# Optimization experiments

Measured on AMD Instinct MI355X. Metric: run time of the kernel, lower is better.

The kernel has to match this reference:

```python
import jax, jax.numpy as jnp
import numpy as np

EPS = 1e-5
K = 20

def knn_idx(x, k):
    # x: (B, N, C) -> (B, N, k) indices of k nearest neighbors (negative sq-dist top-k, self included)
    sq = jnp.sum(x * x, axis=-1)                      # (B, N)
    inner = jnp.einsum('bnc,bmc->bnm', x, x)          # (B, N, N)
    neg_dist = 2.0 * inner - sq[:, :, None] - sq[:, None, :]
    _, idx = jax.lax.top_k(neg_dist, k)
    return idx

def edge_conv(x, w, g, b, m, v, k):
    # x: (B, N, C); w: (O, 2C); BN eval-mode params over O
    idx = knn_idx(x, k)                               # (B, N, k)
    nb = jax.vmap(lambda f, i: f[i])(x, idx)          # (B, N, k, C)
    ctr = x[:, :, None, :]
    e = jnp.concatenate([nb - ctr, jnp.broadcast_to(ctr, nb.shape)], axis=-1)  # (B,N,k,2C)
    h = jnp.einsum('bnkc,oc->bnko', e, w)
    h = (h - m) * jax.lax.rsqrt(v + EPS) * g + b
    h = jnp.where(h > 0, h, 0.2 * h)                  # LeakyReLU(0.2)
    return jnp.max(h, axis=2)                         # (B, N, O)

def conv1d_bn_relu(x, w, bias, g, bt, m, v):
    h = jnp.einsum('bnc,oc->bno', x, w) + bias
    h = (h - m) * jax.lax.rsqrt(v + EPS) * g + bt
    return jax.nn.relu(h)

def setup_inputs() -> dict:
    key = jax.random.key(0)
    ks = jax.random.split(key, 16)
    B, N = 2, 4096
    d = {'x': jax.random.normal(ks[0], (B, N, 3), dtype=jnp.float32)}
    dims = [(3, 64), (64, 64), (64, 128), (128, 256)]
    for i, (ci, co) in enumerate(dims, start=1):
        d[f'w{i}'] = jax.random.normal(ks[i], (co, 2 * ci), dtype=jnp.float32) * 0.05
        d[f'g{i}'] = jnp.ones((co,), jnp.float32)
        d[f'bt{i}'] = jnp.zeros((co,), jnp.float32)
        d[f'm{i}'] = jnp.zeros((co,), jnp.float32)
        d[f'v{i}'] = jnp.ones((co,), jnp.float32)
    head = [(512, 256), (256, 128)]
    for i, (ci, co) in enumerate(head, start=1):
        d[f'hw{i}'] = jax.random.normal(ks[8 + i], (co, ci), dtype=jnp.float32) * 0.05
        d[f'hb{i}'] = jnp.zeros((co,), jnp.float32)
        d[f'hg{i}'] = jnp.ones((co,), jnp.float32)
        d[f'hbt{i}'] = jnp.zeros((co,), jnp.float32)
        d[f'hm{i}'] = jnp.zeros((co,), jnp.float32)
        d[f'hv{i}'] = jnp.ones((co,), jnp.float32)
    d['hw3'] = jax.random.normal(ks[12], (1, 128), dtype=jnp.float32) * 0.05
    d['hb3'] = jnp.zeros((1,), jnp.float32)
    return d

def reference(x, w1, g1, bt1, m1, v1, w2, g2, bt2, m2, v2, w3, g3, bt3, m3, v3,
              w4, g4, bt4, m4, v4,
              hw1, hb1, hg1, hbt1, hm1, hv1, hw2, hb2, hg2, hbt2, hm2, hv2, hw3, hb3):
    x1 = edge_conv(x, w1, g1, bt1, m1, v1, K)   # (B, N, 64)
    x2 = edge_conv(x1, w2, g2, bt2, m2, v2, K)  # (B, N, 64)
    x3 = edge_conv(x2, w3, g3, bt3, m3, v3, K)  # (B, N, 128)
    x4 = edge_conv(x3, w4, g4, bt4, m4, v4, K)  # (B, N, 256)
    xc = jnp.concatenate([x1, x2, x3, x4], axis=-1)  # (B, N, 512)
    h = conv1d_bn_relu(xc, hw1, hb1, hg1, hbt1, hm1, hv1)
    h = conv1d_bn_relu(h, hw2, hb2, hg2, hbt2, hm2, hv2)
    out = jnp.einsum('bnc,oc->bno', h, hw3) + hb3    # (B, N, 1)
    return out[..., 0]                               # (B, N)
```

## Files before the change

kernel.cpp:

```cpp
#include <hip/hip_runtime.h>

#define NPTS 4096
#define EPSF 1e-5f

__device__ __forceinline__ unsigned f2u(float f) {
  unsigned b = __float_as_uint(f);
  return (b & 0x80000000u) ? ~b : (b | 0x80000000u);
}
__device__ __forceinline__ float u2f(unsigned u) {
  unsigned b = (u & 0x80000000u) ? (u & 0x7fffffffu) : ~u;
  return __uint_as_float(b);
}
__device__ __forceinline__ unsigned shflx(unsigned v, int j) {
  return (unsigned)__shfl_xor((int)v, j);
}
__device__ __forceinline__ unsigned long long shflx64(unsigned long long v, int j) {
  unsigned lo = (unsigned)__shfl_xor((int)(unsigned)(v & 0xffffffffull), j);
  unsigned hi = (unsigned)__shfl_xor((int)(unsigned)(v >> 32), j);
  return ((unsigned long long)hi << 32) | lo;
}

__device__ __forceinline__ unsigned sort64_u32(unsigned v, int lane) {
#pragma unroll
  for (int k = 2; k <= 64; k <<= 1) {
#pragma unroll
    for (int j = k >> 1; j >= 1; j >>= 1) {
      unsigned ov = shflx(v, j);
      bool kmin = ((lane & j) == 0) == ((lane & k) == 0);
      v = kmin ? (v < ov ? v : ov) : (v > ov ? v : ov);
    }
  }
  return v;
}

__device__ __forceinline__ void sort128_u32(unsigned& a, unsigned& b, int lane) {
#pragma unroll
  for (int k = 2; k <= 128; k <<= 1) {
#pragma unroll
    for (int j = k >> 1; j >= 1; j >>= 1) {
      if (j == 64) {
        unsigned mn = a < b ? a : b, mx = a < b ? b : a;
        a = mn; b = mx;
      } else {
        unsigned oa = shflx(a, j), ob = shflx(b, j);
        bool lower = (lane & j) == 0;
        bool asca, ascb;
        if (k == 128) { asca = true; ascb = true; }
        else if (k == 64) { asca = true; ascb = false; }
        else { asca = ((lane & k) == 0); ascb = asca; }
        a = (lower == asca) ? (a < oa ? a : oa) : (a > oa ? a : oa);
        b = (lower == ascb) ? (b < ob ? b : ob) : (b > ob ? b : ob);
      }
    }
  }
}

__device__ __forceinline__ unsigned long long sort64_u64(unsigned long long v, int lane) {
#pragma unroll
  for (int k = 2; k <= 64; k <<= 1) {
#pragma unroll
    for (int j = k >> 1; j >= 1; j >>= 1) {
      unsigned long long ov = shflx64(v, j);
      bool kmin = ((lane & j) == 0) == ((lane & k) == 0);
      v = kmin ? (v < ov ? v : ov) : (v > ov ? v : ov);
    }
  }
  return v;
}

__device__ __forceinline__ void sort128_u64(unsigned long long& a, unsigned long long& b,
                                            int lane) {
#pragma unroll
  for (int k = 2; k <= 128; k <<= 1) {
#pragma unroll
    for (int j = k >> 1; j >= 1; j >>= 1) {
      if (j == 64) {
        unsigned long long mn = a < b ? a : b, mx = a < b ? b : a;
        a = mn; b = mx;
      } else {
        unsigned long long oa = shflx64(a, j), ob = shflx64(b, j);
        bool lower = (lane & j) == 0;
        bool asca, ascb;
        if (k == 128) { asca = true; ascb = true; }
        else if (k == 64) { asca = true; ascb = false; }
        else { asca = ((lane & k) == 0); ascb = asca; }
        a = (lower == asca) ? (a < oa ? a : oa) : (a > oa ? a : oa);
        b = (lower == ascb) ? (b < ob ? b : ob) : (b > ob ? b : ob);
      }
    }
  }
}

struct TopkShared {
  unsigned wv[80];
  unsigned ck[128];
  int      ci[128];
  int      cnt_s;
  int      selm[20];
  float    part[4 * 256];
  float    fcv[80];
  int      fcm[80];
};

__device__ __forceinline__ void topk_select(float v[16], TopkShared& sh,
                                            int tid, int lane, int wid) {
  float M = v[0];
#pragma unroll
  for (int j = 1; j < 16; ++j) M = fmaxf(M, v[j]);

  unsigned mk = sort64_u32(f2u(M), lane);

  if (tid == 0) sh.cnt_s = 0;
  if (lane >= 44) sh.wv[wid * 20 + (63 - lane)] = mk;
  __syncthreads();

  unsigned a0 = sh.wv[lane];
  unsigned b0 = (lane < 16) ? sh.wv[64 + lane] : 0u;
  sort128_u32(a0, b0, lane);
  unsigned T0k = (unsigned)__shfl((int)b0, 44);
  float T0f = u2f(T0k);

#pragma unroll
  for (int j = 0; j < 16; ++j) {
    bool pred = (v[j] >= T0f);
    unsigned long long m = __ballot(pred);
    int below = __popcll(m & ((1ull << lane) - 1ull));
    int cw = __popcll(m);
    int base = 0;
    if (lane == 0 && cw) base = atomicAdd(&sh.cnt_s, cw);
    base = __shfl(base, 0);
    if (pred) {
      int pos = base + below;
      if (pos < 128) { sh.ck[pos] = f2u(v[j]); sh.ci[pos] = j * 256 + tid; }
    }
  }
  __syncthreads();
  const int cnt = sh.cnt_s;

  if (cnt <= 128) {
    unsigned long long k0 = (lane < cnt)
        ? (((unsigned long long)sh.ck[lane] << 32) | (unsigned)(~sh.ci[lane])) : 0ull;
    if (cnt <= 64) {
      k0 = sort64_u64(k0, lane);
      if (wid == 0 && lane >= 44) sh.selm[63 - lane] = (int)(~(unsigned)k0);
    } else {
      unsigned long long k1 = (64 + lane < cnt)
          ? (((unsigned long long)sh.ck[64 + lane] << 32) | (unsigned)(~sh.ci[64 + lane]))
          : 0ull;
      sort128_u64(k0, k1, lane);
      if (wid == 0 && lane >= 44) sh.selm[63 - lane] = (int)(~(unsigned)k1);
    }
  } else {
    for (int it = 0; it < 20; ++it) {
      float bv = v[0]; int bj = 0;
#pragma unroll
      for (int j = 1; j < 16; ++j)
        if (v[j] > bv) { bv = v[j]; bj = j; }
      int bm = bj * 256 + tid;
#pragma unroll
      for (int off = 1; off < 64; off <<= 1) {
        float ov = __shfl_xor(bv, off);
        int om = __shfl_xor(bm, off);
        if (ov > bv || (ov == bv && om < bm)) { bv = ov; bm = om; }
      }
      if (lane == 0) { sh.fcv[wid * 20 + it] = bv; sh.fcm[wid * 20 + it] = bm; }
      if ((bm & 255) == tid) v[bm >> 8] = -3.0e38f;
    }
    __syncthreads();
    if (wid == 0) {
      float c0 = sh.fcv[lane]; int m0 = sh.fcm[lane];
      float c1 = (lane < 16) ? sh.fcv[64 + lane] : -3.0e38f;
      int   m1 = (lane < 16) ? sh.fcm[64 + lane] : 0x7fffffff;
      for (int it = 0; it < 20; ++it) {
        float bv; int bm, bs;
        if (c0 > c1 || (c0 == c1 && m0 < m1)) { bv = c0; bm = m0; bs = lane; }
        else { bv = c1; bm = m1; bs = 64 + lane; }
#pragma unroll
        for (int off = 1; off < 64; off <<= 1) {
          float ov = __shfl_xor(bv, off);
          int om = __shfl_xor(bm, off);
          int os = __shfl_xor(bs, off);
          if (ov > bv || (ov == bv && om < bm)) { bv = ov; bm = om; bs = os; }
        }
        if (lane == 0) sh.selm[it] = bm;
        if (bs == lane) c0 = -3.0e38f;
        else if (bs == 64 + lane) c1 = -3.0e38f;
      }
    }
  }
  __syncthreads();
}

__device__ __forceinline__ void topk_gather(const TopkShared& sh, TopkShared& shm,
                                            const float* __restrict__ P,
                                            const float* __restrict__ Q,
                                            float* __restrict__ Y, int ldy, int O,
                                            int bBase, int n, int tid, int lane, int wid) {
  for (int o = lane; o < O; o += 64) {
    float q = Q[(size_t)(bBase + n) * O + o];
    float best = -3.0e38f;
#pragma unroll
    for (int kk = 0; kk < 5; ++kk) {
      int s = sh.selm[wid * 5 + kk];
      float t = P[(size_t)(bBase + s) * O + o] + q;
      t = t > 0.f ? t : 0.2f * t;
      best = fmaxf(best, t);
    }
    shm.part[wid * 256 + o] = best;
  }
  __syncthreads();
  for (int o = tid; o < O; o += 256) {
    float b2 = fmaxf(fmaxf(shm.part[o], shm.part[256 + o]),
                     fmaxf(shm.part[512 + o], shm.part[768 + o]));
    Y[(size_t)(bBase + n) * ldy + o] = b2;
  }
}

__global__ void fold_edge_k(const float* __restrict__ w, const float* __restrict__ g,
                            const float* __restrict__ bt, const float* __restrict__ m,
                            const float* __restrict__ v, int O, int C,
                            float* __restrict__ wdf, float* __restrict__ wqf,
                            float* __restrict__ c0) {
  int t = blockIdx.x * 256 + threadIdx.x;
  if (t >= O * C) return;
  int o = t / C, c = t - o * C;
  float A = g[o] * (1.0f / sqrtf(v[o] + EPSF));
  float wd = w[o * 2 * C + c], wc = w[o * 2 * C + C + c];
  wdf[t] = A * wd;
  wqf[t] = A * (wc - wd);
  if (c == 0) c0[o] = bt[o] - m[o] * A;
}

__global__ void fold_head_k(const float* __restrict__ hw, const float* __restrict__ hb,
                            const float* __restrict__ hg, const float* __restrict__ hbt,
                            const float* __restrict__ hm, const float* __restrict__ hv,
                            int O, int C, float* __restrict__ hwf, float* __restrict__ cb) {
  int t = blockIdx.x * 256 + threadIdx.x;
  if (t >= O * C) return;
  int o = t / C, c = t - o * C;
  float A = hg[o] * (1.0f / sqrtf(hv[o] + EPSF));
  hwf[t] = A * hw[t];
  if (c == 0) cb[o] = (hb[o] - hm[o]) * A + hbt[o];
}

__global__ void sq_k(const float* __restrict__ X, int lda, int C,
                     float* __restrict__ sq, int nrows) {
  int r = blockIdx.x * 256 + threadIdx.x;
  if (r >= nrows) return;
  const float* p = X + (size_t)r * lda;
  float s = 0.f;
  for (int c = 0; c < C; ++c) s += p[c] * p[c];
  sq[r] = s;
}

__global__ void pq3_k(const float* __restrict__ x, const float* __restrict__ wdf,
                      const float* __restrict__ wqf, const float* __restrict__ c0,
                      float* __restrict__ P, float* __restrict__ Q) {
  int t = blockIdx.x * 256 + threadIdx.x;
  int r = t >> 6, o = t & 63;
  float x0 = x[r * 3], x1 = x[r * 3 + 1], x2 = x[r * 3 + 2];
  P[(size_t)r * 64 + o] = x0 * wdf[o * 3] + x1 * wdf[o * 3 + 1] + x2 * wdf[o * 3 + 2];
  Q[(size_t)r * 64 + o] = x0 * wqf[o * 3] + x1 * wqf[o * 3 + 1] + x2 * wqf[o * 3 + 2] + c0[o];
}

__global__ void dist3_k(const float* __restrict__ xb, const float* __restrict__ sqb,
                        float* __restrict__ D, int r0) {
  int t = blockIdx.x * 256 + threadIdx.x;
  int rl = t >> 12;
  int mc = t & (NPTS - 1);
  int n = r0 + rl;
  float x0 = xb[n * 3], x1 = xb[n * 3 + 1], x2 = xb[n * 3 + 2];
  float y0 = xb[mc * 3], y1 = xb[mc * 3 + 1], y2 = xb[mc * 3 + 2];
  float inner = x0 * y0 + x1 * y1 + x2 * y2;
  D[(size_t)rl * NPTS + mc] = 2.0f * inner - sqb[n] - sqb[mc];
}

__global__ __launch_bounds__(256) void topk_l1_fused(
    const float* __restrict__ x, const float* __restrict__ sqg,
    const float* __restrict__ P, const float* __restrict__ Q,
    float* __restrict__ Y, int ldy) {
  const int tid = threadIdx.x;
  const int lane = tid & 63, wid = tid >> 6;
  const int n = blockIdx.x;
  const int bBase = blockIdx.y * NPTS;
  const float* xb = x + (size_t)bBase * 3;
  const float* sqb = sqg + bBase;

  __shared__ TopkShared sh;

  float xn0 = xb[n * 3], xn1 = xb[n * 3 + 1], xn2 = xb[n * 3 + 2];
  float sn = sqb[n];
  float v[16];
#pragma unroll
  for (int j = 0; j < 16; ++j) {
    int mc = j * 256 + tid;
    float y0 = xb[mc * 3], y1 = xb[mc * 3 + 1], y2 = xb[mc * 3 + 2];
    float inner = xn0 * y0 + xn1 * y1 + xn2 * y2;
    v[j] = 2.0f * inner - sn - sqb[mc];
  }

  topk_select(v, sh, tid, lane, wid);
  topk_gather(sh, sh, P, Q, Y, ldy, 64, bBase, n, tid, lane, wid);
}

__global__ __launch_bounds__(256) void dist_sym_k(
    const float* __restrict__ X0, int lda, int C,
    const float* __restrict__ sq0, float* __restrict__ D0) {
  int t = blockIdx.x;
  int bi = 0;
  while (t >= 32 - bi) { t -= 32 - bi; ++bi; }
  const int bj = bi + t;
  const int b = blockIdx.y;
  const float* X = X0 + (size_t)b * NPTS * lda;
  const float* sq = sq0 + (size_t)b * NPTS;
  float* D = D0 + (size_t)b * NPTS * NPTS;

  const int row0 = bi * 128, col0 = bj * 128;
  const int tid = threadIdx.x;
  const int tx = tid & 15, ty = tid >> 4;

  __shared__ float As[16 * 132];
  __shared__ float Bs[16 * 132];

  const int lr = tid >> 1;
  const int lc = (tid & 1) * 8;
  const float* Ap = X + (size_t)(row0 + lr) * lda + lc;
  const float* Bp = X + (size_t)(col0 + lr) * lda + lc;

  float acc[8][8] = {};
  for (int c0 = 0; c0 < C; c0 += 16) {
    float4 a0 = *(const float4*)(Ap + c0);
    float4 a1 = *(const float4*)(Ap + c0 + 4);
    float4 b0 = *(const float4*)(Bp + c0);
    float4 b1 = *(const float4*)(Bp + c0 + 4);
    __syncthreads();
    As[(lc + 0) * 132 + lr] = a0.x; As[(lc + 1) * 132 + lr] = a0.y;
    As[(lc + 2) * 132 + lr] = a0.z; As[(lc + 3) * 132 + lr] = a0.w;
    As[(lc + 4) * 132 + lr] = a1.x; As[(lc + 5) * 132 + lr] = a1.y;
    As[(lc + 6) * 132 + lr] = a1.z; As[(lc + 7) * 132 + lr] = a1.w;
    Bs[(lc + 0) * 132 + lr] = b0.x; Bs[(lc + 1) * 132 + lr] = b0.y;
    Bs[(lc + 2) * 132 + lr] = b0.z; Bs[(lc + 3) * 132 + lr] = b0.w;
    Bs[(lc + 4) * 132 + lr] = b1.x; Bs[(lc + 5) * 132 + lr] = b1.y;
    Bs[(lc + 6) * 132 + lr] = b1.z; Bs[(lc + 7) * 132 + lr] = b1.w;
    __syncthreads();
#pragma unroll
    for (int c = 0; c < 16; ++c) {
      float4 av0 = *(const float4*)&As[c * 132 + ty * 8];
      float4 av1 = *(const float4*)&As[c * 132 + ty * 8 + 4];
      float4 bv0 = *(const float4*)&Bs[c * 132 + tx * 8];
      float4 bv1 = *(const float4*)&Bs[c * 132 + tx * 8 + 4];
      float aa[8] = {av0.x, av0.y, av0.z, av0.w, av1.x, av1.y, av1.z, av1.w};
      float bb[8] = {bv0.x, bv0.y, bv0.z, bv0.w, bv1.x, bv1.y, bv1.z, bv1.w};
#pragma unroll
      for (int i = 0; i < 8; ++i)
#pragma unroll
        for (int j = 0; j < 8; ++j) acc[i][j] = fmaf(aa[i], bb[j], acc[i][j]);
    }
  }

  float rs[8], cs[8];
#pragma unroll
  for (int i = 0; i < 8; ++i) rs[i] = sq[row0 + ty * 8 + i];
#pragma unroll
  for (int j = 0; j < 8; ++j) cs[j] = sq[col0 + tx * 8 + j];

#pragma unroll
  for (int i = 0; i < 8; ++i) {
    const int row = row0 + ty * 8 + i;
    float vals[8];
#pragma unroll
    for (int j = 0; j < 8; ++j) vals[j] = (2.0f * acc[i][j] - rs[i]) - cs[j];
    *(float4*)&D[(size_t)row * NPTS + col0 + tx * 8] =
        make_float4(vals[0], vals[1], vals[2], vals[3]);
    *(float4*)&D[(size_t)row * NPTS + col0 + tx * 8 + 4] =
        make_float4(vals[4], vals[5], vals[6], vals[7]);
  }

  if (bi != bj) {
#pragma unroll
    for (int j = 0; j < 8; ++j) {
      const int col = col0 + tx * 8 + j;
      float mv[8];
#pragma unroll
      for (int i = 0; i < 8; ++i) mv[i] = (2.0f * acc[i][j] - cs[j]) - rs[i];
      *(float4*)&D[(size_t)col * NPTS + row0 + ty * 8] =
          make_float4(mv[0], mv[1], mv[2], mv[3]);
      *(float4*)&D[(size_t)col * NPTS + row0 + ty * 8 + 4] =
          make_float4(mv[4], mv[5], mv[6], mv[7]);
    }
  }
}

template <int EPI>
__global__ __launch_bounds__(256) void gemm_nt(
    const float* __restrict__ A, int lda,
    const float* __restrict__ Bm, int ldb,
    float* __restrict__ Out, int ldo, int C,
    const float* __restrict__ sqA, const float* __restrict__ sqB,
    const float* __restrict__ bias) {
  __shared__ __align__(16) float As[16][68];
  __shared__ __align__(16) float Bs[16][68];
  const int tx = threadIdx.x, ty = threadIdx.y;
  const int tid = ty * 16 + tx;
  const int row0 = blockIdx.y * 64, col0 = blockIdx.x * 64;
  const int lr = tid >> 2;
  const int lc = (tid & 3) << 2;
  const float* Ap = A + (size_t)(row0 + lr) * lda + lc;
  const float* Bp = Bm + (size_t)(col0 + lr) * ldb + lc;
  float acc[4][4] = {};
  for (int c0 = 0; c0 < C; c0 += 16) {
    float4 av = *(const float4*)(Ap + c0);
    float4 bv = *(const float4*)(Bp + c0);
    As[lc + 0][lr] = av.x; As[lc + 1][lr] = av.y;
    As[lc + 2][lr] = av.z; As[lc + 3][lr] = av.w;
    Bs[lc + 0][lr] = bv.x; Bs[lc + 1][lr] = bv.y;
    Bs[lc + 2][lr] = bv.z; Bs[lc + 3][lr] = bv.w;
    __syncthreads();
#pragma unroll
    for (int c = 0; c < 16; ++c) {
      float4 a4 = *(const float4*)(&As[c][ty << 2]);
      float4 b4 = *(const float4*)(&Bs[c][tx << 2]);
      float aa[4] = {a4.x, a4.y, a4.z, a4.w};
      float bb[4] = {b4.x, b4.y, b4.z, b4.w};
#pragma unroll
      for (int i = 0; i < 4; ++i)
#pragma unroll
        for (int j = 0; j < 4; ++j) acc[i][j] = fmaf(aa[i], bb[j], acc[i][j]);
    }
    __syncthreads();
  }
  const int row = row0 + (ty << 2), col = col0 + (tx << 2);
#pragma unroll
  for (int i = 0; i < 4; ++i) {
    float vals[4];
#pragma unroll
    for (int j = 0; j < 4; ++j) {
      float va = acc[i][j];
      if (EPI == 0) vals[j] = va;
      else if (EPI == 1) vals[j] = va + bias[col + j];
      else if (EPI == 2) vals[j] = 2.0f * va - sqA[row + i] - sqB[col + j];
      else { float t = va + bias[col + j]; vals[j] = t > 0.f ? t : 0.f; }
    }
    *(float4*)(&Out[(size_t)(row + i) * ldo + col]) =
        make_float4(vals[0], vals[1], vals[2], vals[3]);
  }
}

__global__ __launch_bounds__(256) void topk_max_f32(
    const float* __restrict__ D, long long dStride,
    const float* __restrict__ P, const float* __restrict__ Q,
    float* __restrict__ Y, int ldy, int O, int bBase0, int r0) {
  const int tid = threadIdx.x;
  const int lane = tid & 63, wid = tid >> 6;
  const int nloc = blockIdx.x;
  const int n = r0 + nloc;
  const int bBase = bBase0 + blockIdx.y * NPTS;
  const float* drow = D + (size_t)blockIdx.y * (size_t)dStride + (size_t)nloc * NPTS;

  __shared__ TopkShared sh;

  float v[16];
#pragma unroll
  for (int j = 0; j < 16; ++j) v[j] = drow[j * 256 + tid];

  topk_select(v, sh, tid, lane, wid);
  topk_gather(sh, sh, P, Q, Y, ldy, O, bBase, n, tid, lane, wid);
}

__global__ void final_dot_k(const float* __restrict__ h2, const float* __restrict__ w3,
                            const float* __restrict__ b3, float* __restrict__ out) {
  int gt = blockIdx.x * 256 + threadIdx.x;
  int row = gt >> 6, lane = gt & 63;
  float s = h2[(size_t)row * 128 + lane] * w3[lane] +
            h2[(size_t)row * 128 + 64 + lane] * w3[64 + lane];
#pragma unroll
  for (int off = 32; off > 0; off >>= 1) s += __shfl_down(s, off);
  if (lane == 0) out[row] = s + b3[0];
}

extern "C" void kernel_launch(void* const* d_in, const int* in_sizes, int n_in,
                              void* d_out, int out_size, void* d_ws, size_t ws_size,
                              hipStream_t stream) {
  const int B = 2, N = NPTS;
  const size_t NN = (size_t)N * N;
  const float* x = (const float*)d_in[0];
  const float* w[4]  = {(const float*)d_in[1], (const float*)d_in[6],
                        (const float*)d_in[11], (const float*)d_in[16]};
  const float* g[4]  = {(const float*)d_in[2], (const float*)d_in[7],
                        (const float*)d_in[12], (const float*)d_in[17]};
  const float* bt[4] = {(const float*)d_in[3], (const float*)d_in[8],
                        (const float*)d_in[13], (const float*)d_in[18]};
  const float* mm[4] = {(const float*)d_in[4], (const float*)d_in[9],
                        (const float*)d_in[14], (const float*)d_in[19]};
  const float* vv[4] = {(const float*)d_in[5], (const float*)d_in[10],
                        (const float*)d_in[15], (const float*)d_in[20]};
  const float* hw1 = (const float*)d_in[21]; const float* hb1 = (const float*)d_in[22];
  const float* hg1 = (const float*)d_in[23]; const float* hbt1 = (const float*)d_in[24];
  const float* hm1 = (const float*)d_in[25]; const float* hv1 = (const float*)d_in[26];
  const float* hw2 = (const float*)d_in[27]; const float* hb2 = (const float*)d_in[28];
  const float* hg2 = (const float*)d_in[29]; const float* hbt2 = (const float*)d_in[30];
  const float* hm2 = (const float*)d_in[31]; const float* hv2 = (const float*)d_in[32];
  const float* hw3 = (const float*)d_in[33]; const float* hb3 = (const float*)d_in[34];
  float* out = (float*)d_out;

  char* wsb = (char*)d_ws;
  size_t off = 0;
  auto alloc = [&](size_t nbytes) {
    char* p = wsb + off;
    off += (nbytes + 255) & ~(size_t)255;
    return p;
  };
  float* xc   = (float*)alloc((size_t)B * N * 512 * 4);
  float* P    = (float*)alloc((size_t)B * N * 256 * 4);
  float* Q    = (float*)alloc((size_t)B * N * 256 * 4);
  float* sq   = (float*)alloc((size_t)B * N * 4);
  float* wdf  = (float*)alloc(256 * 256 * 4);
  float* wqf  = (float*)alloc(256 * 256 * 4);
  float* c0   = (float*)alloc(256 * 4);
  float* hwf1 = (float*)alloc(256 * 512 * 4);
  float* cb1  = (float*)alloc(256 * 4);
  float* hwf2 = (float*)alloc(128 * 256 * 4);
  float* cb2  = (float*)alloc(128 * 4);
  float* D    = (float*)(wsb + off);
  size_t avail = (ws_size > off) ? (ws_size - off) : 0;
  const bool merged = (avail >= (size_t)B * NN * 4);
  int rows_tile = 4096;
  if (!merged)
    while ((size_t)rows_tile * N * 4 > avail && rows_tile > 64) rows_tile >>= 1;

  const int Cin[4]  = {3, 64, 64, 128};
  const int Oc[4]   = {64, 64, 128, 256};
  const int ioff[4] = {0, 0, 64, 128};
  const int ooff[4] = {0, 64, 128, 256};
  dim3 blk2(16, 16);

  for (int L = 0; L < 4; ++L) {
    const int C = Cin[L], O = Oc[L];
    const float* in = (L == 0) ? x : (xc + ioff[L]);
    const int lda = (L == 0) ? 3 : 512;

    fold_edge_k<<<dim3((O * C + 255) / 256), dim3(256), 0, stream>>>(
        w[L], g[L], bt[L], mm[L], vv[L], O, C, wdf, wqf, c0);
    sq_k<<<dim3((B * N + 255) / 256), dim3(256), 0, stream>>>(in, lda, C, sq, B * N);
    if (L == 0) {
      pq3_k<<<dim3(B * N * 64 / 256), dim3(256), 0, stream>>>(x, wdf, wqf, c0, P, Q);
    } else {
      gemm_nt<0><<<dim3(O / 64, B * N / 64), blk2, 0, stream>>>(
          in, lda, wdf, C, P, O, C, nullptr, nullptr, nullptr);
      gemm_nt<1><<<dim3(O / 64, B * N / 64), blk2, 0, stream>>>(
          in, lda, wqf, C, Q, O, C, nullptr, nullptr, c0);
    }

    if (merged) {
      if (L == 0) {
        topk_l1_fused<<<dim3(N, B), dim3(256), 0, stream>>>(
            x, sq, P, Q, xc + ooff[0], 512);
      } else {
        dist_sym_k<<<dim3(528, B), dim3(256), 0, stream>>>(in, lda, C, sq, D);
        topk_max_f32<<<dim3(N, B), dim3(256), 0, stream>>>(
            D, (long long)NN, P, Q, xc + ooff[L], 512, O, 0, 0);
      }
      continue;
    }

    for (int b = 0; b < B; ++b) {
      for (int r0 = 0; r0 < N; r0 += rows_tile) {
        if (L == 0) {
          dist3_k<<<dim3((unsigned)((size_t)rows_tile * N / 256)), dim3(256), 0, stream>>>(
              x + (size_t)b * N * 3, sq + b * N, D, r0);
        } else {
          gemm_nt<2><<<dim3(N / 64, rows_tile / 64), blk2, 0, stream>>>(
              in + ((size_t)b * N + r0) * lda, lda, in + (size_t)b * N * lda, lda,
              D, N, C, sq + b * N + r0, sq + b * N, nullptr);
        }
        topk_max_f32<<<dim3(rows_tile, 1), dim3(256), 0, stream>>>(
            D, 0, P, Q, xc + ooff[L], 512, O, b * N, r0);
      }
    }
  }

  fold_head_k<<<dim3((256 * 512 + 255) / 256), dim3(256), 0, stream>>>(
      hw1, hb1, hg1, hbt1, hm1, hv1, 256, 512, hwf1, cb1);
  fold_head_k<<<dim3((128 * 256 + 255) / 256), dim3(256), 0, stream>>>(
      hw2, hb2, hg2, hbt2, hm2, hv2, 128, 256, hwf2, cb2);

  float* h1 = P;
  float* h2 = Q;
  gemm_nt<3><<<dim3(256 / 64, B * N / 64), blk2, 0, stream>>>(
      xc, 512, hwf1, 512, h1, 256, 512, nullptr, nullptr, cb1);
  gemm_nt<3><<<dim3(128 / 64, B * N / 64), blk2, 0, stream>>>(
      h1, 256, hwf2, 256, h2, 128, 256, nullptr, nullptr, cb2);
  final_dot_k<<<dim3(B * N / 4), dim3(256), 0, stream>>>(h2, hw3, hb3, out);
}
```

Measured before the change: 700.8 us.

## Fuse distance GEMM with streaming top-k for C=64 layers, then merge candidates

For the two edge-conv layers whose input has 64 channels, the full N×N distance matrix is no longer written to memory. A tiled kernel computes distances for 32 rows against a 512-column chunk, keeps a per-row candidate list in shared memory filtered by a running 20th-best threshold, and writes 20 candidates per chunk. A merge kernel then reduces the 8 chunks to the final 20 neighbours and performs the gather-and-max. This removes the D-matrix write and re-read, at the cost of more ballot and sort work and a candidate buffer. It also removes the L0 dist3 fallback path.

```diff
diff --git a/kernel.cpp b/kernel.cpp
--- a/kernel.cpp
+++ b/kernel.cpp
@@ -17,6 +17,11 @@
 __device__ __forceinline__ unsigned long long shflx64(unsigned long long v, int j) {
   unsigned lo = (unsigned)__shfl_xor((int)(unsigned)(v & 0xffffffffull), j);
   unsigned hi = (unsigned)__shfl_xor((int)(unsigned)(v >> 32), j);
+  return ((unsigned long long)hi << 32) | lo;
+}
+__device__ __forceinline__ unsigned long long bcast64(unsigned long long v, int src) {
+  unsigned lo = (unsigned)__shfl((int)(unsigned)(v & 0xffffffffull), src);
+  unsigned hi = (unsigned)__shfl((int)(unsigned)(v >> 32), src);
   return ((unsigned long long)hi << 32) | lo;
 }
 
@@ -263,18 +268,6 @@
   Q[(size_t)r * 64 + o] = x0 * wqf[o * 3] + x1 * wqf[o * 3 + 1] + x2 * wqf[o * 3 + 2] + c0[o];
 }
 
-__global__ void dist3_k(const float* __restrict__ xb, const float* __restrict__ sqb,
-                        float* __restrict__ D, int r0) {
-  int t = blockIdx.x * 256 + threadIdx.x;
-  int rl = t >> 12;
-  int mc = t & (NPTS - 1);
-  int n = r0 + rl;
-  float x0 = xb[n * 3], x1 = xb[n * 3 + 1], x2 = xb[n * 3 + 2];
-  float y0 = xb[mc * 3], y1 = xb[mc * 3 + 1], y2 = xb[mc * 3 + 2];
-  float inner = x0 * y0 + x1 * y1 + x2 * y2;
-  D[(size_t)rl * NPTS + mc] = 2.0f * inner - sqb[n] - sqb[mc];
-}
-
 __global__ __launch_bounds__(256) void topk_l1_fused(
     const float* __restrict__ x, const float* __restrict__ sqg,
     const float* __restrict__ P, const float* __restrict__ Q,
@@ -301,6 +294,172 @@
 
   topk_select(v, sh, tid, lane, wid);
   topk_gather(sh, sh, P, Q, Y, ldy, 64, bBase, n, tid, lane, wid);
+}
+
+#define KG_RB 32
+__global__ __launch_bounds__(256) void knn_group_c64(
+    const float* __restrict__ X0, int lda, const float* __restrict__ sq0,
+    unsigned long long* __restrict__ cand) {
+  const int tid = threadIdx.x;
+  const int lane = tid & 63, wid = tid >> 6;
+  const int txc = tid & 31;
+  const int tr  = tid >> 5;
+  const int rbase = blockIdx.x * KG_RB;
+  const int cbase = blockIdx.y * 512;
+  const int b = blockIdx.z;
+  const float* X = X0 + (size_t)b * NPTS * lda;
+  const float* sq = sq0 + (size_t)b * NPTS;
+
+  __shared__ float AsT[64 * 36];
+  __shared__ float BsT[64 * 68];
+  __shared__ unsigned long long lst[KG_RB][104];
+  __shared__ float rsq[KG_RB];
+
+  if (tid < KG_RB) rsq[tid] = sq[rbase + tid];
+
+  int rcnt[4] = {0, 0, 0, 0};
+  unsigned long long rtk[4] = {0ull, 0ull, 0ull, 0ull};
+
+#pragma unroll
+  for (int k = 0; k < 2; ++k) {
+    int id = tid + 256 * k;
+    int r = id >> 4, q = id & 15;
+    float4 f = *(const float4*)(X + (size_t)(rbase + r) * lda + q * 4);
+    AsT[(q * 4 + 0) * 36 + r] = f.x;
+    AsT[(q * 4 + 1) * 36 + r] = f.y;
+    AsT[(q * 4 + 2) * 36 + r] = f.z;
+    AsT[(q * 4 + 3) * 36 + r] = f.w;
+  }
+
+  const unsigned long long hmask =
+      (lane < 32) ? 0x00000000FFFFFFFFull : 0xFFFFFFFF00000000ull;
+  const unsigned long long below = (1ull << lane) - 1ull;
+  const int rowbase = wid * 8;
+
+  for (int st = 0; st < 8; ++st) {
+    const int c0 = cbase + st * 64;
+    __syncthreads();
+#pragma unroll
+    for (int k = 0; k < 4; ++k) {
+      int id = tid + 256 * k;
+      int m = id >> 4, q = id & 15;
+      float4 f = *(const float4*)(X + (size_t)(c0 + m) * lda + q * 4);
+      BsT[(q * 4 + 0) * 68 + m] = f.x;
+      BsT[(q * 4 + 1) * 68 + m] = f.y;
+      BsT[(q * 4 + 2) * 68 + m] = f.z;
+      BsT[(q * 4 + 3) * 68 + m] = f.w;
+    }
+    __syncthreads();
+
+    float acc[4][2] = {};
+#pragma unroll 4
+    for (int c = 0; c < 64; ++c) {
+      float4 a4 = *(const float4*)&AsT[c * 36 + tr * 4];
+      float2 b2 = *(const float2*)&BsT[c * 68 + txc * 2];
+      float aa[4] = {a4.x, a4.y, a4.z, a4.w};
+      float bb[2] = {b2.x, b2.y};
+#pragma unroll
+      for (int i = 0; i < 4; ++i)
+#pragma unroll
+        for (int j = 0; j < 2; ++j) acc[i][j] = fmaf(aa[i], bb[j], acc[i][j]);
+    }
+
+    float2 cs2 = *(const float2*)(sq + c0 + txc * 2);
+    float csq[2] = {cs2.x, cs2.y};
+
+#pragma unroll
+    for (int i = 0; i < 4; ++i) {
+      const int rl = tr * 4 + i;
+#pragma unroll
+      for (int j = 0; j < 2; ++j) {
+        float v = (2.0f * acc[i][j] - rsq[rl]) - csq[j];
+        int gcol = c0 + txc * 2 + j;
+        unsigned long long key =
+            ((unsigned long long)f2u(v) << 32) | (unsigned)(~gcol);
+        bool pred = key > rtk[i];
+        unsigned long long bm = __ballot(pred);
+        unsigned long long sub = bm & hmask;
+        if (pred) lst[rl][rcnt[i] + (int)__popcll(sub & below)] = key;
+        rcnt[i] += (int)__popcll(sub);
+      }
+    }
+
+#pragma unroll
+    for (int rr = 0; rr < 8; ++rr) {
+      const int rl = rowbase + rr;
+      int c2 = __shfl(rcnt[rr & 3], (rr & 4) ? 32 : 0);
+      if (c2 > 40) {
+        unsigned long long k0 = (lane < c2) ? lst[rl][lane] : 0ull;
+        unsigned long long k1 = (64 + lane < c2) ? lst[rl][64 + lane] : 0ull;
+        sort128_u64(k0, k1, lane);
+        if (lane >= 44) lst[rl][63 - lane] = k1;
+        unsigned long long t20 = bcast64(k1, 44);
+        if ((lane >> 5) == (rr >> 2)) {
+          rcnt[rr & 3] = 20;
+          rtk[rr & 3] = t20;
+        }
+      }
+    }
+  }
+
+#pragma unroll
+  for (int rr = 0; rr < 8; ++rr) {
+    const int rl = rowbase + rr;
+    int c2 = __shfl(rcnt[rr & 3], (rr & 4) ? 32 : 0);
+    unsigned long long k0 = (lane < c2) ? lst[rl][lane] : 0ull;
+    unsigned long long k1 = (64 + lane < c2) ? lst[rl][64 + lane] : 0ull;
+    sort128_u64(k0, k1, lane);
+    if (lane >= 44)
+      cand[((size_t)(b * NPTS + rbase + rl) * 8 + blockIdx.y) * 20 + (63 - lane)] = k1;
+  }
+}
+
+__global__ __launch_bounds__(256) void knn_merge(
+    const unsigned long long* __restrict__ cand,
+    const float* __restrict__ P, const float* __restrict__ Q,
+    float* __restrict__ Y, int ldy, int O) {
+  const int tid = threadIdx.x, lane = tid & 63, wid = tid >> 6;
+  const int n = blockIdx.x;
+  const int bBase = blockIdx.y * NPTS;
+
+  __shared__ unsigned long long ck[80];
+  __shared__ int selm[20];
+  __shared__ float part[4 * 256];
+
+  unsigned long long k0 = 0ull;
+  if (lane < 40) {
+    int g = 2 * wid + (lane >= 20);
+    int kk = (lane >= 20) ? lane - 20 : lane;
+    k0 = cand[((size_t)(bBase + n) * 8 + g) * 20 + kk];
+  }
+  k0 = sort64_u64(k0, lane);
+  if (lane >= 44) ck[wid * 20 + (63 - lane)] = k0;
+  __syncthreads();
+
+  unsigned long long a0 = ck[lane];
+  unsigned long long a1 = (lane < 16) ? ck[64 + lane] : 0ull;
+  sort128_u64(a0, a1, lane);
+  if (wid == 0 && lane >= 44) selm[63 - lane] = (int)(~(unsigned)a1) & (NPTS - 1);
+  __syncthreads();
+
+  for (int o = lane; o < O; o += 64) {
+    float q = Q[(size_t)(bBase + n) * O + o];
+    float best = -3.0e38f;
+#pragma unroll
+    for (int kk = 0; kk < 5; ++kk) {
+      int s = selm[wid * 5 + kk];
+      float t = P[(size_t)(bBase + s) * O + o] + q;
+      t = t > 0.f ? t : 0.2f * t;
+      best = fmaxf(best, t);
+    }
+    part[wid * 256 + o] = best;
+  }
+  __syncthreads();
+  for (int o = tid; o < O; o += 256) {
+    float b2 = fmaxf(fmaxf(part[o], part[256 + o]),
+                     fmaxf(part[512 + o], part[768 + o]));
+    Y[(size_t)(bBase + n) * ldy + o] = b2;
+  }
 }
 
 __global__ __launch_bounds__(256) void dist_sym_k(
@@ -521,6 +680,8 @@
   float* cb1  = (float*)alloc(256 * 4);
   float* hwf2 = (float*)alloc(128 * 256 * 4);
   float* cb2  = (float*)alloc(128 * 4);
+  unsigned long long* cand =
+      (unsigned long long*)alloc((size_t)B * N * 8 * 20 * 8);
   float* D    = (float*)(wsb + off);
   size_t avail = (ws_size > off) ? (ws_size - off) : 0;
   const bool merged = (avail >= (size_t)B * NN * 4);
@@ -551,28 +712,29 @@
           in, lda, wqf, C, Q, O, C, nullptr, nullptr, c0);
     }
 
+    if (L == 0) {
+      topk_l1_fused<<<dim3(N, B), dim3(256), 0, stream>>>(
+          x, sq, P, Q, xc + ooff[0], 512);
+      continue;
+    }
+    if (C == 64) {
+      knn_group_c64<<<dim3(N / KG_RB, 8, B), dim3(256), 0, stream>>>(
+          in, 512, sq, cand);
+      knn_merge<<<dim3(N, B), dim3(256), 0, stream>>>(
+          cand, P, Q, xc + ooff[L], 512, O);
+      continue;
+    }
     if (merged) {
-      if (L == 0) {
-        topk_l1_fused<<<dim3(N, B), dim3(256), 0, stream>>>(
-            x, sq, P, Q, xc + ooff[0], 512);
-      } else {
-        dist_sym_k<<<dim3(528, B), dim3(256), 0, stream>>>(in, lda, C, sq, D);
-        topk_max_f32<<<dim3(N, B), dim3(256), 0, stream>>>(
-            D, (long long)NN, P, Q, xc + ooff[L], 512, O, 0, 0);
-      }
+      dist_sym_k<<<dim3(528, B), dim3(256), 0, stream>>>(in, lda, C, sq, D);
+      topk_max_f32<<<dim3(N, B), dim3(256), 0, stream>>>(
+          D, (long long)NN, P, Q, xc + ooff[L], 512, O, 0, 0);
       continue;
     }
-
     for (int b = 0; b < B; ++b) {
       for (int r0 = 0; r0 < N; r0 += rows_tile) {
-        if (L == 0) {
-          dist3_k<<<dim3((unsigned)((size_t)rows_tile * N / 256)), dim3(256), 0, stream>>>(
-              x + (size_t)b * N * 3, sq + b * N, D, r0);
-        } else {
-          gemm_nt<2><<<dim3(N / 64, rows_tile / 64), blk2, 0, stream>>>(
-              in + ((size_t)b * N + r0) * lda, lda, in + (size_t)b * N * lda, lda,
-              D, N, C, sq + b * N + r0, sq + b * N, nullptr);
-        }
+        gemm_nt<2><<<dim3(N / 64, rows_tile / 64), blk2, 0, stream>>>(
+            in + ((size_t)b * N + r0) * lda, lda, in + (size_t)b * N * lda, lda,
+            D, N, C, sq + b * N + r0, sq + b * N, nullptr);
         topk_max_f32<<<dim3(rows_tile, 1), dim3(256), 0, stream>>>(
             D, 0, P, Q, xc + ooff[L], 512, O, b * N, r0);
       }
```

Measured after the change: 1.552 ms. 121% more time.
